# Performance work log

Hardware: AMD Instinct MI355X
Metric: run time of the kernel (lower is better)

## Reference

```python
import jax, jax.numpy as jnp
import numpy as np

D = 1024
H = 16
DH = D // H  # 64
EPS = 1e-6


def setup_inputs() -> dict:
    key = jax.random.key(0)
    ks = jax.random.split(key, 12)
    B, Nq, Nk = 4, 2048, 2048
    s = 1.0 / np.sqrt(D)
    return {
        "x": jax.random.normal(ks[0], (B, Nq, D), dtype=jnp.float32),
        "context": jax.random.normal(ks[1], (B, Nk, D), dtype=jnp.float32),
        "Wq": jax.random.normal(ks[2], (D, D), dtype=jnp.float32) * s,
        "bq": jnp.zeros((D,), dtype=jnp.float32),
        "Wk": jax.random.normal(ks[3], (D, D), dtype=jnp.float32) * s,
        "bk": jnp.zeros((D,), dtype=jnp.float32),
        "Wv": jax.random.normal(ks[4], (D, D), dtype=jnp.float32) * s,
        "bv": jnp.zeros((D,), dtype=jnp.float32),
        "Wo": jax.random.normal(ks[5], (D, D), dtype=jnp.float32) * s,
        "bo": jnp.zeros((D,), dtype=jnp.float32),
    }


def _split_heads(t):
    B, N, _ = t.shape
    return t.reshape(B, N, H, DH).transpose(0, 2, 1, 3)  # (B,H,N,DH)


def reference(x, context, Wq, bq, Wk, bk, Wv, bv, Wo, bo):
    B, Nq, _ = x.shape
    # QKV projections (torch Linear: x @ W.T + b)
    q = _split_heads(x @ Wq.T + bq)          # (B,H,Nq,DH)
    k = _split_heads(context @ Wk.T + bk)    # (B,H,Nk,DH)
    v = _split_heads(context @ Wv.T + bv)    # (B,H,Nk,DH)
    # QK-norm (use_qk_norm=True), scale buffer = 1.0
    q = q / (jnp.linalg.norm(q, axis=-1, keepdims=True) + EPS)
    k = k / (jnp.linalg.norm(k, axis=-1, keepdims=True) + EPS)
    scale = jnp.float32(1.0)
    attn = jnp.einsum("bhqd,bhkd->bhqk", q, k) * scale
    attn = jax.nn.softmax(attn, axis=-1)
    out = jnp.einsum("bhqk,bhkd->bhqd", attn, v)  # (B,H,Nq,DH)
    out = out.transpose(0, 2, 1, 3).reshape(B, Nq, D)
    return out @ Wo.T + bo
```

## Files before the change

### kernel.cpp

```cpp
#include <hip/hip_runtime.h>

typedef unsigned short u16;
typedef unsigned int u32;
typedef __attribute__((ext_vector_type(8))) short bf16x8;
typedef __attribute__((ext_vector_type(4))) float f32x4;
typedef __attribute__((ext_vector_type(16))) float f32x16;
typedef __attribute__((ext_vector_type(4))) u32 u32x4;

#define D_MODEL 1024
#define NHEAD 16
#define DHEAD 64
#define SEQ 2048
#define BATCH 4
#define MTOT (BATCH * SEQ)
#define LOG2E 1.4426950408889634f

#define MFMA16(A, B, C) __builtin_amdgcn_mfma_f32_16x16x32_bf16((A), (B), (C), 0, 0, 0)
#define MFMA32(A, B, C) __builtin_amdgcn_mfma_f32_32x32x16_bf16((A), (B), (C), 0, 0, 0)

__device__ __forceinline__ u16 f2bf(float f) {
  u32 u = __builtin_bit_cast(u32, f);
  u = (u + 0x7FFFu + ((u >> 16) & 1u)) >> 16;
  return (u16)u;
}

__device__ __forceinline__ void async_copy16(void* lds, const void* g) {
  __builtin_amdgcn_global_load_lds(
      (const __attribute__((address_space(1))) u32*)g,
      (__attribute__((address_space(3))) u32*)lds, 16, 0, 0);
}

__device__ __forceinline__ u32 cvtpk_bf16(float lo, float hi) {
  u32 r;
  asm("v_cvt_pk_bf16_f32 %0, %1, %2" : "=v"(r) : "v"(lo), "v"(hi));
  return r;
}
__device__ __forceinline__ void permswap(u32& a, u32& b) {
  asm("v_permlane32_swap_b32 %0, %1" : "+v"(a), "+v"(b));
}

__global__ void cvt2(const float* __restrict__ s0, u16* __restrict__ d0,
                     const float* __restrict__ s1, u16* __restrict__ d1, int n4) {
  int i = blockIdx.x * blockDim.x + threadIdx.x;
  int st = gridDim.x * blockDim.x;
  for (; i < 2 * n4; i += st) {
    const float* s = (i < n4) ? s0 : s1;
    u16* d = (i < n4) ? d0 : d1;
    int j = (i < n4) ? i : (i - n4);
    float4 v = ((const float4*)s)[j];
    ushort4 o;
    o.x = f2bf(v.x); o.y = f2bf(v.y); o.z = f2bf(v.z); o.w = f2bf(v.w);
    ((ushort4*)d)[j] = o;
  }
}

__global__ __launch_bounds__(256, 3) void gemm_qkv(
    const u16* __restrict__ xb, const u16* __restrict__ cb,
    const u16* __restrict__ wqb, const u16* __restrict__ wkvb,
    const float* __restrict__ bq, const float* __restrict__ bk,
    const float* __restrict__ bv,
    u16* __restrict__ Qb, u16* __restrict__ Kb, u16* __restrict__ Vtb) {
  __shared__ u16 As[128 * 64];
  __shared__ u16 Bs[128 * 64];
  const int K = 1024;
  const int tid = threadIdx.x;
  const int l = tid & 63;
  const int wid = tid >> 6;
  const int bid = blockIdx.x;
  const int swz = (bid & 7) * 192 + (bid >> 3);
  const bool isQ = swz < 512;
  const u16* A;
  const u16* Bw;
  int m0, n0;
  if (isQ) {
    A = xb; Bw = wqb;
    m0 = (swz >> 3) * 128;
    n0 = (swz & 7) * 128;
  } else {
    const int s = swz - 512;
    A = cb; Bw = wkvb;
    m0 = (s >> 4) * 128;
    n0 = (s & 15) * 128;
  }
  const int wr = wid >> 1, wc = wid & 1;
  const int r = l & 15, kg = l >> 4;
  f32x4 acc[4][4] = {};
  char* AsB = (char*)As;
  char* BsB = (char*)Bs;
  const int arow = l >> 3;
  const int agran = (l & 7) ^ arow;

  for (int kt = 0; kt < K; kt += 64) {
#pragma unroll
    for (int cc = 0; cc < 4; ++cc) {
      int c = wid + (cc << 2);
      int rowi = (c << 3) + arow;
      const char* ga = (const char*)A + ((size_t)(m0 + rowi) * K + kt) * 2 + agran * 16;
      async_copy16(AsB + c * 1024, ga);
      const char* gb = (const char*)Bw + ((size_t)(n0 + rowi) * K + kt) * 2 + agran * 16;
      async_copy16(BsB + c * 1024, gb);
    }
    __syncthreads();
#pragma unroll
    for (int half = 0; half < 2; ++half) {
      const int g = ((half << 2) + kg) ^ (r & 7);
      bf16x8 af[4], bf[4];
#pragma unroll
      for (int i = 0; i < 4; ++i) {
        af[i] = *(const bf16x8*)(AsB + (wr * 64 + i * 16 + r) * 128 + g * 16);
        bf[i] = *(const bf16x8*)(BsB + (wc * 64 + i * 16 + r) * 128 + g * 16);
      }
#pragma unroll
      for (int i = 0; i < 4; ++i)
#pragma unroll
        for (int j = 0; j < 4; ++j)
          acc[i][j] = MFMA16(af[i], bf[j], acc[i][j]);
    }
    __syncthreads();
  }

  const int colbase = n0 + wc * 64;
  const bool isV = (!isQ) && (colbase >= 1024);
  if (!isV) {
    u16* C = isQ ? Qb : Kb;
    const float* bias = isQ ? bq : bk;
    const float sMul = isQ ? LOG2E : 1.0f;
    float bvj[4];
#pragma unroll
    for (int j = 0; j < 4; ++j) bvj[j] = bias[colbase + j * 16 + r];
#pragma unroll
    for (int i = 0; i < 4; ++i) {
      const int row0 = m0 + wr * 64 + i * 16 + kg * 4;
#pragma unroll
      for (int jj = 0; jj < 4; ++jj) {
        float t[4];
        float s2 = 0.f;
#pragma unroll
        for (int j = 0; j < 4; ++j) {
          t[j] = acc[i][j][jj] + bvj[j];
          s2 += t[j] * t[j];
        }
        s2 += __shfl_xor(s2, 1);
        s2 += __shfl_xor(s2, 2);
        s2 += __shfl_xor(s2, 4);
        s2 += __shfl_xor(s2, 8);
        const float inv = sMul / (sqrtf(s2) + 1e-6f);
#pragma unroll
        for (int j = 0; j < 4; ++j)
          C[(size_t)(row0 + jj) * D_MODEL + colbase + j * 16 + r] = f2bf(t[j] * inv);
      }
    }
  } else {
#pragma unroll
    for (int i = 0; i < 4; ++i) {
#pragma unroll
      for (int j = 0; j < 4; ++j) {
        const int col = colbase + j * 16 + r;
        const float bvv = bv[col - 1024];
        const int row0 = m0 + wr * 64 + i * 16 + kg * 4;
        const int hh = (col - 1024) >> 6, dh = col & 63;
        const int bb = row0 >> 11, tok = row0 & 2047;
        ushort4 o;
        o.x = f2bf(acc[i][j][0] + bvv);
        o.y = f2bf(acc[i][j][1] + bvv);
        o.z = f2bf(acc[i][j][2] + bvv);
        o.w = f2bf(acc[i][j][3] + bvv);
        *(ushort4*)(Vtb + ((size_t)((bb * 16 + hh) * 64 + dh) * SEQ + tok)) = o;
      }
    }
  }
}

__global__ __launch_bounds__(256, 3) void gemm_out(const u16* __restrict__ A,
                                                   const u16* __restrict__ Bw,
                                                   const float* __restrict__ bias,
                                                   float* __restrict__ Cout) {
  __shared__ u16 As[128 * 64];
  __shared__ u16 Bs[128 * 64];
  const int K = 1024, N = 1024;
  const int tid = threadIdx.x;
  const int l = tid & 63;
  const int wid = tid >> 6;
  const int bid = blockIdx.x;
  const int swz = (bid & 7) * 64 + (bid >> 3);
  const int m0 = (swz >> 3) * 128;
  const int n0 = (swz & 7) * 128;
  const int wr = wid >> 1, wc = wid & 1;
  const int r = l & 15, kg = l >> 4;
  f32x4 acc[4][4] = {};
  char* AsB = (char*)As;
  char* BsB = (char*)Bs;
  const int arow = l >> 3;
  const int agran = (l & 7) ^ arow;

  for (int kt = 0; kt < K; kt += 64) {
#pragma unroll
    for (int cc = 0; cc < 4; ++cc) {
      int c = wid + (cc << 2);
      int rowi = (c << 3) + arow;
      const char* ga = (const char*)A + ((size_t)(m0 + rowi) * K + kt) * 2 + agran * 16;
      async_copy16(AsB + c * 1024, ga);
      const char* gb = (const char*)Bw + ((size_t)(n0 + rowi) * K + kt) * 2 + agran * 16;
      async_copy16(BsB + c * 1024, gb);
    }
    __syncthreads();
#pragma unroll
    for (int half = 0; half < 2; ++half) {
      const int g = ((half << 2) + kg) ^ (r & 7);
      bf16x8 af[4], bf[4];
#pragma unroll
      for (int i = 0; i < 4; ++i) {
        af[i] = *(const bf16x8*)(AsB + (wr * 64 + i * 16 + r) * 128 + g * 16);
        bf[i] = *(const bf16x8*)(BsB + (wc * 64 + i * 16 + r) * 128 + g * 16);
      }
#pragma unroll
      for (int i = 0; i < 4; ++i)
#pragma unroll
        for (int j = 0; j < 4; ++j)
          acc[i][j] = MFMA16(af[i], bf[j], acc[i][j]);
    }
    __syncthreads();
  }
#pragma unroll
  for (int i = 0; i < 4; ++i) {
#pragma unroll
    for (int j = 0; j < 4; ++j) {
      const int col = n0 + wc * 64 + j * 16 + r;
      const float bvv = bias[col];
      const int row0 = m0 + wr * 64 + i * 16 + kg * 4;
#pragma unroll
      for (int jj = 0; jj < 4; ++jj)
        Cout[(size_t)(row0 + jj) * N + col] = acc[i][j][jj] + bvv;
    }
  }
}

#define KVB 64
#define NT (SEQ / KVB)

__global__ __launch_bounds__(256, 4) void attn_kernel(const u16* __restrict__ Q,
                                                      const u16* __restrict__ K,
                                                      const u16* __restrict__ Vt,
                                                      u16* __restrict__ O) {
  __shared__ alignas(16) u16 Ks[2][KVB * 64];
  __shared__ alignas(16) u16 Vs[2][64 * KVB];
  const int tid = threadIdx.x;
  const int l = tid & 63;
  const int wid = tid >> 6;
  const int qg = l & 31;
  const int half = l >> 5;
  const int bid = blockIdx.x;
  const int swz = (bid & 7) * 128 + (bid >> 3);
  const int qt = swz & 15;
  const int bh = swz >> 4;
  const int b = bh >> 4, h = bh & 15;

  const int srow = l >> 3, slot = l & 7;
  const int r0 = (wid << 3) + srow;
  const int r1 = ((wid + 4) << 3) + srow;
  const int sw0 = (r0 ^ (r0 >> 3)) & 7;
  const int sw1 = (r1 ^ (r1 >> 3)) & 7;
  const u16* pK0 = K + ((size_t)(b * SEQ) + r0) * D_MODEL + h * 64 + (slot ^ sw0) * 8;
  const u16* pK1 = K + ((size_t)(b * SEQ) + r1) * D_MODEL + h * 64 + (slot ^ sw1) * 8;
  const u16* pV0 = Vt + ((size_t)(bh * 64) + r0) * SEQ + (slot ^ sw0) * 8;
  const u16* pV1 = Vt + ((size_t)(bh * 64) + r1) * SEQ + (slot ^ sw1) * 8;
  const int ldsc0 = wid * 1024, ldsc1 = (wid + 4) * 1024;

  bf16x8 qf[4];
  {
    const u16* q0 = Q + ((size_t)(b * SEQ + qt * 128 + wid * 32 + qg)) * D_MODEL + h * 64 + half * 8;
#pragma unroll
    for (int dc = 0; dc < 4; ++dc) qf[dc] = *(const bf16x8*)(q0 + dc * 16);
  }
  f32x16 oacc[2] = {};
  float lrun = 0.f;

  auto stage = [&](int bufi) {
    char* KsX = (char*)Ks[bufi];
    char* VsX = (char*)Vs[bufi];
    async_copy16(KsX + ldsc0, pK0);
    async_copy16(KsX + ldsc1, pK1);
    async_copy16(VsX + ldsc0, pV0);
    async_copy16(VsX + ldsc1, pV1);
    pK0 += (size_t)KVB * D_MODEL;
    pK1 += (size_t)KVB * D_MODEL;
    pV0 += KVB;
    pV1 += KVB;
  };

  stage(0);
  __syncthreads();
  int buf = 0;

  for (int t = 0; t < NT; ++t) {
    if (t + 1 < NT) stage(buf ^ 1);
    const char* KsC = (const char*)Ks[buf];
    const char* VsC = (const char*)Vs[buf];

    f32x16 st[2] = {};
    __builtin_amdgcn_s_setprio(1);
#pragma unroll
    for (int t32 = 0; t32 < 2; ++t32) {
      const int rowK = t32 * 32 + qg;
      const int swk = (rowK ^ (rowK >> 3)) & 7;
#pragma unroll
      for (int dc = 0; dc < 4; ++dc) {
        const int p = (dc * 2 + half) ^ swk;
        bf16x8 kf = *(const bf16x8*)(KsC + rowK * 128 + p * 16);
        st[t32] = MFMA32(kf, qf[dc], st[t32]);
      }
    }
    __builtin_amdgcn_s_setprio(0);

    float rs0 = 0.f, rs1 = 0.f, rs2 = 0.f, rs3 = 0.f;
#pragma unroll
    for (int t32 = 0; t32 < 2; ++t32)
#pragma unroll
      for (int rr = 0; rr < 16; rr += 4) {
        float p0 = __builtin_amdgcn_exp2f(st[t32][rr + 0]);
        float p1 = __builtin_amdgcn_exp2f(st[t32][rr + 1]);
        float p2 = __builtin_amdgcn_exp2f(st[t32][rr + 2]);
        float p3 = __builtin_amdgcn_exp2f(st[t32][rr + 3]);
        st[t32][rr + 0] = p0; st[t32][rr + 1] = p1;
        st[t32][rr + 2] = p2; st[t32][rr + 3] = p3;
        rs0 += p0; rs1 += p1; rs2 += p2; rs3 += p3;
      }
    lrun += (rs0 + rs1) + (rs2 + rs3);

#pragma unroll
    for (int t32 = 0; t32 < 2; ++t32) {
#pragma unroll
      for (int cc = 0; cc < 2; ++cc) {
        const int base = cc * 8;
        u32 wA = cvtpk_bf16(st[t32][base + 0], st[t32][base + 1]);
        u32 wB = cvtpk_bf16(st[t32][base + 2], st[t32][base + 3]);
        u32 wC = cvtpk_bf16(st[t32][base + 4], st[t32][base + 5]);
        u32 wD = cvtpk_bf16(st[t32][base + 6], st[t32][base + 7]);
        permswap(wA, wC);
        permswap(wB, wD);
        u32x4 pw = {wA, wB, wC, wD};
        bf16x8 pf = __builtin_bit_cast(bf16x8, pw);
        const int qw = ((t32 * 2 + cc) << 1) + half;
        __builtin_amdgcn_s_setprio(1);
#pragma unroll
        for (int dt = 0; dt < 2; ++dt) {
          const int rowV = dt * 32 + qg;
          const int pp = qw ^ ((rowV ^ (rowV >> 3)) & 7);
          bf16x8 vf = *(const bf16x8*)(VsC + rowV * 128 + pp * 16);
          oacc[dt] = MFMA32(vf, pf, oacc[dt]);
        }
        __builtin_amdgcn_s_setprio(0);
      }
    }
    __syncthreads();
    buf ^= 1;
  }

  lrun += __shfl_xor(lrun, 32);
  const float inv = 1.0f / lrun;
  u32* orow = (u32*)(O + ((size_t)(b * SEQ + qt * 128 + wid * 32 + qg)) * D_MODEL + h * 64);
#pragma unroll
  for (int dt = 0; dt < 2; ++dt)
#pragma unroll
    for (int w = 0; w < 8; ++w) {
      const int dh = dt * 32 + (w & 1) * 2 + 8 * (w >> 1) + 4 * half;
      u32 pk = cvtpk_bf16(oacc[dt][2 * w] * inv, oacc[dt][2 * w + 1] * inv);
      orow[dh >> 1] = pk;
    }
}

extern "C" void kernel_launch(void* const* d_in, const int* in_sizes, int n_in,
                              void* d_out, int out_size, void* d_ws, size_t ws_size,
                              hipStream_t stream) {
  const float* x   = (const float*)d_in[0];
  const float* ctx = (const float*)d_in[1];
  const float* Wq  = (const float*)d_in[2];
  const float* bq  = (const float*)d_in[3];
  const float* Wk  = (const float*)d_in[4];
  const float* bk  = (const float*)d_in[5];
  const float* Wv  = (const float*)d_in[6];
  const float* bv  = (const float*)d_in[7];
  const float* Wo  = (const float*)d_in[8];
  const float* bo  = (const float*)d_in[9];
  float* out = (float*)d_out;

  const size_t NTOK = (size_t)MTOT * D_MODEL;
  const size_t WSZ = (size_t)D_MODEL * D_MODEL;
  u16* xb  = (u16*)d_ws;
  u16* cb  = xb + NTOK;
  u16* wqb = cb + NTOK;
  u16* wkb = wqb + WSZ;
  u16* wvb = wkb + WSZ;
  u16* wob = wvb + WSZ;
  u16* Qb  = wob + WSZ;
  u16* Kb  = Qb + NTOK;
  u16* Vtb = Kb + NTOK;
  (void)in_sizes; (void)n_in; (void)out_size; (void)ws_size;

  dim3 blk(256);
  cvt2<<<2048, blk, 0, stream>>>(x, xb, ctx, cb, (int)(NTOK / 4));
  cvt2<<<512, blk, 0, stream>>>(Wq, wqb, Wk, wkb, (int)(WSZ / 4));
  cvt2<<<512, blk, 0, stream>>>(Wv, wvb, Wo, wob, (int)(WSZ / 4));

  gemm_qkv<<<1536, blk, 0, stream>>>(xb, cb, wqb, wkb, bq, bk, bv, Qb, Kb, Vtb);

  attn_kernel<<<1024, blk, 0, stream>>>(Qb, Kb, Vtb, xb);

  gemm_out<<<512, blk, 0, stream>>>(xb, wob, bo, out);
}
```

Baseline: 182.3 us.

## Process two 32-row query groups per wave in attention to reuse K/V fragments

Each wave now handles 64 query rows (two 32-row groups) instead of 32, so each block covers 256 queries and the grid halves to 512 blocks. Every K and V fragment read from LDS feeds two MFMAs, halving LDS traffic and global K/V staging per query. The cost is more registers for accumulators and Q fragments, with launch bounds relaxed to 2 blocks per SM, and fewer blocks in the grid, which lowers occupancy and parallelism.

```diff
diff --git a/kernel.cpp b/kernel.cpp
--- a/kernel.cpp
+++ b/kernel.cpp
@@ -238,7 +238,7 @@
 #define KVB 64
 #define NT (SEQ / KVB)
 
-__global__ __launch_bounds__(256, 4) void attn_kernel(const u16* __restrict__ Q,
+__global__ __launch_bounds__(256, 2) void attn_kernel(const u16* __restrict__ Q,
                                                       const u16* __restrict__ K,
                                                       const u16* __restrict__ Vt,
                                                       u16* __restrict__ O) {
@@ -250,9 +250,9 @@
   const int qg = l & 31;
   const int half = l >> 5;
   const int bid = blockIdx.x;
-  const int swz = (bid & 7) * 128 + (bid >> 3);
-  const int qt = swz & 15;
-  const int bh = swz >> 4;
+  const int swz = (bid & 7) * 64 + (bid >> 3);
+  const int qt = swz & 7;
+  const int bh = swz >> 3;
   const int b = bh >> 4, h = bh & 15;
 
   const int srow = l >> 3, slot = l & 7;
@@ -266,14 +266,17 @@
   const u16* pV1 = Vt + ((size_t)(bh * 64) + r1) * SEQ + (slot ^ sw1) * 8;
   const int ldsc0 = wid * 1024, ldsc1 = (wid + 4) * 1024;
 
-  bf16x8 qf[4];
+  bf16x8 qf[2][4];
   {
-    const u16* q0 = Q + ((size_t)(b * SEQ + qt * 128 + wid * 32 + qg)) * D_MODEL + h * 64 + half * 8;
-#pragma unroll
-    for (int dc = 0; dc < 4; ++dc) qf[dc] = *(const bf16x8*)(q0 + dc * 16);
-  }
-  f32x16 oacc[2] = {};
-  float lrun = 0.f;
+    const u16* q0 = Q + ((size_t)(b * SEQ + qt * 256 + wid * 64 + qg)) * D_MODEL + h * 64 + half * 8;
+#pragma unroll
+    for (int g = 0; g < 2; ++g)
+#pragma unroll
+      for (int dc = 0; dc < 4; ++dc)
+        qf[g][dc] = *(const bf16x8*)(q0 + g * 32 * D_MODEL + dc * 16);
+  }
+  f32x16 oacc[2][2] = {};
+  float lr0 = 0.f, lr1 = 0.f;
 
   auto stage = [&](int bufi) {
     char* KsX = (char*)Ks[bufi];
@@ -297,7 +300,7 @@
     const char* KsC = (const char*)Ks[buf];
     const char* VsC = (const char*)Vs[buf];
 
-    f32x16 st[2] = {};
+    f32x16 s0[2] = {}, s1[2] = {};
     __builtin_amdgcn_s_setprio(1);
 #pragma unroll
     for (int t32 = 0; t32 < 2; ++t32) {
@@ -307,39 +310,64 @@
       for (int dc = 0; dc < 4; ++dc) {
         const int p = (dc * 2 + half) ^ swk;
         bf16x8 kf = *(const bf16x8*)(KsC + rowK * 128 + p * 16);
-        st[t32] = MFMA32(kf, qf[dc], st[t32]);
+        s0[t32] = MFMA32(kf, qf[0][dc], s0[t32]);
+        s1[t32] = MFMA32(kf, qf[1][dc], s1[t32]);
       }
     }
     __builtin_amdgcn_s_setprio(0);
 
-    float rs0 = 0.f, rs1 = 0.f, rs2 = 0.f, rs3 = 0.f;
-#pragma unroll
-    for (int t32 = 0; t32 < 2; ++t32)
-#pragma unroll
-      for (int rr = 0; rr < 16; rr += 4) {
-        float p0 = __builtin_amdgcn_exp2f(st[t32][rr + 0]);
-        float p1 = __builtin_amdgcn_exp2f(st[t32][rr + 1]);
-        float p2 = __builtin_amdgcn_exp2f(st[t32][rr + 2]);
-        float p3 = __builtin_amdgcn_exp2f(st[t32][rr + 3]);
-        st[t32][rr + 0] = p0; st[t32][rr + 1] = p1;
-        st[t32][rr + 2] = p2; st[t32][rr + 3] = p3;
-        rs0 += p0; rs1 += p1; rs2 += p2; rs3 += p3;
-      }
-    lrun += (rs0 + rs1) + (rs2 + rs3);
+    {
+      float a0 = 0.f, a1 = 0.f, a2 = 0.f, a3 = 0.f;
+#pragma unroll
+      for (int t32 = 0; t32 < 2; ++t32)
+#pragma unroll
+        for (int rr = 0; rr < 16; rr += 4) {
+          float p0 = __builtin_amdgcn_exp2f(s0[t32][rr + 0]);
+          float p1 = __builtin_amdgcn_exp2f(s0[t32][rr + 1]);
+          float p2 = __builtin_amdgcn_exp2f(s0[t32][rr + 2]);
+          float p3 = __builtin_amdgcn_exp2f(s0[t32][rr + 3]);
+          s0[t32][rr + 0] = p0; s0[t32][rr + 1] = p1;
+          s0[t32][rr + 2] = p2; s0[t32][rr + 3] = p3;
+          a0 += p0; a1 += p1; a2 += p2; a3 += p3;
+        }
+      lr0 += (a0 + a1) + (a2 + a3);
+      float c0 = 0.f, c1 = 0.f, c2 = 0.f, c3 = 0.f;
+#pragma unroll
+      for (int t32 = 0; t32 < 2; ++t32)
+#pragma unroll
+        for (int rr = 0; rr < 16; rr += 4) {
+          float p0 = __builtin_amdgcn_exp2f(s1[t32][rr + 0]);
+          float p1 = __builtin_amdgcn_exp2f(s1[t32][rr + 1]);
+          float p2 = __builtin_amdgcn_exp2f(s1[t32][rr + 2]);
+          float p3 = __builtin_amdgcn_exp2f(s1[t32][rr + 3]);
+          s1[t32][rr + 0] = p0; s1[t32][rr + 1] = p1;
+          s1[t32][rr + 2] = p2; s1[t32][rr + 3] = p3;
+          c0 += p0; c1 += p1; c2 += p2; c3 += p3;
+        }
+      lr1 += (c0 + c1) + (c2 + c3);
+    }
 
 #pragma unroll
     for (int t32 = 0; t32 < 2; ++t32) {
 #pragma unroll
       for (int cc = 0; cc < 2; ++cc) {
         const int base = cc * 8;
-        u32 wA = cvtpk_bf16(st[t32][base + 0], st[t32][base + 1]);
-        u32 wB = cvtpk_bf16(st[t32][base + 2], st[t32][base + 3]);
-        u32 wC = cvtpk_bf16(st[t32][base + 4], st[t32][base + 5]);
-        u32 wD = cvtpk_bf16(st[t32][base + 6], st[t32][base + 7]);
-        permswap(wA, wC);
-        permswap(wB, wD);
-        u32x4 pw = {wA, wB, wC, wD};
-        bf16x8 pf = __builtin_bit_cast(bf16x8, pw);
+        u32 wA0 = cvtpk_bf16(s0[t32][base + 0], s0[t32][base + 1]);
+        u32 wB0 = cvtpk_bf16(s0[t32][base + 2], s0[t32][base + 3]);
+        u32 wC0 = cvtpk_bf16(s0[t32][base + 4], s0[t32][base + 5]);
+        u32 wD0 = cvtpk_bf16(s0[t32][base + 6], s0[t32][base + 7]);
+        permswap(wA0, wC0);
+        permswap(wB0, wD0);
+        u32x4 pw0 = {wA0, wB0, wC0, wD0};
+        bf16x8 pf0 = __builtin_bit_cast(bf16x8, pw0);
+        u32 wA1 = cvtpk_bf16(s1[t32][base + 0], s1[t32][base + 1]);
+        u32 wB1 = cvtpk_bf16(s1[t32][base + 2], s1[t32][base + 3]);
+        u32 wC1 = cvtpk_bf16(s1[t32][base + 4], s1[t32][base + 5]);
+        u32 wD1 = cvtpk_bf16(s1[t32][base + 6], s1[t32][base + 7]);
+        permswap(wA1, wC1);
+        permswap(wB1, wD1);
+        u32x4 pw1 = {wA1, wB1, wC1, wD1};
+        bf16x8 pf1 = __builtin_bit_cast(bf16x8, pw1);
         const int qw = ((t32 * 2 + cc) << 1) + half;
         __builtin_amdgcn_s_setprio(1);
 #pragma unroll
@@ -347,7 +375,8 @@
           const int rowV = dt * 32 + qg;
           const int pp = qw ^ ((rowV ^ (rowV >> 3)) & 7);
           bf16x8 vf = *(const bf16x8*)(VsC + rowV * 128 + pp * 16);
-          oacc[dt] = MFMA32(vf, pf, oacc[dt]);
+          oacc[0][dt] = MFMA32(vf, pf0, oacc[0][dt]);
+          oacc[1][dt] = MFMA32(vf, pf1, oacc[1][dt]);
         }
         __builtin_amdgcn_s_setprio(0);
       }
@@ -356,16 +385,21 @@
     buf ^= 1;
   }
 
-  lrun += __shfl_xor(lrun, 32);
-  const float inv = 1.0f / lrun;
-  u32* orow = (u32*)(O + ((size_t)(b * SEQ + qt * 128 + wid * 32 + qg)) * D_MODEL + h * 64);
+  lr0 += __shfl_xor(lr0, 32);
+  lr1 += __shfl_xor(lr1, 32);
+  const float inv0 = 1.0f / lr0;
+  const float inv1 = 1.0f / lr1;
+  u32* orow0 = (u32*)(O + ((size_t)(b * SEQ + qt * 256 + wid * 64 + qg)) * D_MODEL + h * 64);
+  u32* orow1 = (u32*)((u16*)orow0 + (size_t)32 * D_MODEL);
 #pragma unroll
   for (int dt = 0; dt < 2; ++dt)
 #pragma unroll
     for (int w = 0; w < 8; ++w) {
       const int dh = dt * 32 + (w & 1) * 2 + 8 * (w >> 1) + 4 * half;
-      u32 pk = cvtpk_bf16(oacc[dt][2 * w] * inv, oacc[dt][2 * w + 1] * inv);
-      orow[dh >> 1] = pk;
+      u32 pk0 = cvtpk_bf16(oacc[0][dt][2 * w] * inv0, oacc[0][dt][2 * w + 1] * inv0);
+      orow0[dh >> 1] = pk0;
+      u32 pk1 = cvtpk_bf16(oacc[1][dt][2 * w] * inv1, oacc[1][dt][2 * w + 1] * inv1);
+      orow1[dh >> 1] = pk1;
     }
 }
 
@@ -404,7 +438,7 @@
 
   gemm_qkv<<<1536, blk, 0, stream>>>(xb, cb, wqb, wkb, bq, bk, bv, Qb, Kb, Vtb);
 
-  attn_kernel<<<1024, blk, 0, stream>>>(Qb, Kb, Vtb, xb);
+  attn_kernel<<<512, blk, 0, stream>>>(Qb, Kb, Vtb, xb);
 
   gemm_out<<<512, blk, 0, stream>>>(xb, wob, bo, out);
 }
```

New measurement: 186.4 us. +2.2%, slower.

## Prefetch two KV tiles ahead in attention and merge conversion kernels

Applied to the files above, without the earlier changes.

The attention loop now issues async copies for two tiles up front and waits with explicit vmcnt counters and raw s_barrier calls, so the next tile's load stays in flight while the current tile is processed instead of relying on __syncthreads. The three fp32-to-bf16 conversion launches are merged into one kernel to cut launch overhead. The manual waitcnt and barrier handling must stay correct for the double buffer, because the restage into a buffer only happens after a barrier that follows its processing.

```diff
diff --git a/kernel.cpp b/kernel.cpp
--- a/kernel.cpp
+++ b/kernel.cpp
@@ -39,14 +39,35 @@
   asm("v_permlane32_swap_b32 %0, %1" : "+v"(a), "+v"(b));
 }
 
-__global__ void cvt2(const float* __restrict__ s0, u16* __restrict__ d0,
-                     const float* __restrict__ s1, u16* __restrict__ d1, int n4) {
+__device__ __forceinline__ void wg_barrier() {
+  __builtin_amdgcn_sched_barrier(0);
+  asm volatile("s_barrier" ::: "memory");
+  __builtin_amdgcn_sched_barrier(0);
+}
+#define VMCNT(N) asm volatile("s_waitcnt vmcnt(" #N ")" ::: "memory")
+
+__global__ void cvt_all(const float* __restrict__ x, const float* __restrict__ ctx,
+                        const float* __restrict__ Wq, const float* __restrict__ Wk,
+                        const float* __restrict__ Wv, const float* __restrict__ Wo,
+                        u16* __restrict__ xb, u16* __restrict__ cb,
+                        u16* __restrict__ wqb, u16* __restrict__ wkb,
+                        u16* __restrict__ wvb, u16* __restrict__ wob) {
+  const int NX = 1 << 21;
+  const int NW = 1 << 18;
+  const int total = 2 * NX + 4 * NW;
   int i = blockIdx.x * blockDim.x + threadIdx.x;
-  int st = gridDim.x * blockDim.x;
-  for (; i < 2 * n4; i += st) {
-    const float* s = (i < n4) ? s0 : s1;
-    u16* d = (i < n4) ? d0 : d1;
-    int j = (i < n4) ? i : (i - n4);
+  const int st = gridDim.x * blockDim.x;
+  for (; i < total; i += st) {
+    const float* s; u16* d; int j;
+    if (i < NX)            { s = x;   d = xb;  j = i; }
+    else if (i < 2 * NX)   { s = ctx; d = cb;  j = i - NX; }
+    else {
+      int k = i - 2 * NX;
+      int wi = k >> 18;
+      j = k & (NW - 1);
+      s = (wi == 0) ? Wq : (wi == 1) ? Wk : (wi == 2) ? Wv : Wo;
+      d = (wi == 0) ? wqb : (wi == 1) ? wkb : (wi == 2) ? wvb : wob;
+    }
     float4 v = ((const float4*)s)[j];
     ushort4 o;
     o.x = f2bf(v.x); o.y = f2bf(v.y); o.z = f2bf(v.z); o.w = f2bf(v.w);
@@ -288,15 +309,9 @@
     pV1 += KVB;
   };
 
-  stage(0);
-  __syncthreads();
-  int buf = 0;
-
-  for (int t = 0; t < NT; ++t) {
-    if (t + 1 < NT) stage(buf ^ 1);
-    const char* KsC = (const char*)Ks[buf];
-    const char* VsC = (const char*)Vs[buf];
-
+  auto process = [&](int bufi) {
+    const char* KsC = (const char*)Ks[bufi];
+    const char* VsC = (const char*)Vs[bufi];
     f32x16 st[2] = {};
     __builtin_amdgcn_s_setprio(1);
 #pragma unroll
@@ -352,9 +367,23 @@
         __builtin_amdgcn_s_setprio(0);
       }
     }
-    __syncthreads();
-    buf ^= 1;
-  }
+  };
+
+  stage(0);
+  stage(1);
+  VMCNT(0);
+  wg_barrier();
+
+  for (int t = 0; t < NT - 1; ++t) {
+    VMCNT(4);
+    wg_barrier();
+    process(t & 1);
+    wg_barrier();
+    if (t + 2 < NT) stage(t & 1);
+  }
+  VMCNT(0);
+  wg_barrier();
+  process((NT - 1) & 1);
 
   lrun += __shfl_xor(lrun, 32);
   const float inv = 1.0f / lrun;
@@ -398,9 +427,7 @@
   (void)in_sizes; (void)n_in; (void)out_size; (void)ws_size;
 
   dim3 blk(256);
-  cvt2<<<2048, blk, 0, stream>>>(x, xb, ctx, cb, (int)(NTOK / 4));
-  cvt2<<<512, blk, 0, stream>>>(Wq, wqb, Wk, wkb, (int)(WSZ / 4));
-  cvt2<<<512, blk, 0, stream>>>(Wv, wvb, Wo, wob, (int)(WSZ / 4));
+  cvt_all<<<2048, blk, 0, stream>>>(x, ctx, Wq, Wk, Wv, Wo, xb, cb, wqb, wkb, wvb, wob);
 
   gemm_qkv<<<1536, blk, 0, stream>>>(xb, cb, wqb, wkb, bq, bk, bv, Qb, Kb, Vtb);
 
```

Measured after the change: 178.7 us. -2.0%, faster.
